# Kernel optimization log

Hardware: AMD Instinct MI355X
Metric: run time of the kernel (lower is better)

## Reference

```python
import jax, jax.numpy as jnp
import numpy as np

N = 50000
E = 800000
TEXT_VOCAB = 7000
ACTION_DIM = 64
MAX_POS = 5120
POS_DIM = 128   # edge encoder out_dim
NODE_DIM = 128  # text_out 64 + type_out 64
EDGE_DIM = 128
H1 = 256
OUT = 32
NEG_SLOPE = 0.2


def _pos_table():
    # sinusoidal table, [MAX_POS+1, POS_DIM]; even cols = cos, odd cols = sin
    positions = np.arange(0, MAX_POS + 1, dtype=np.float32)
    inv_freq = 1.0 / (10000.0 ** (np.arange(0.0, POS_DIM, 2.0, dtype=np.float32) / POS_DIM))
    si = np.outer(positions, inv_freq)
    tab = np.zeros((MAX_POS + 1, POS_DIM), dtype=np.float32)
    tab[:, 1::2] = np.sin(si)
    tab[:, 0::2] = np.cos(si)
    return jnp.asarray(tab)


def setup_inputs() -> dict:
    key = jax.random.key(0)
    ks = jax.random.split(key, 32)
    ri = jax.random.randint
    nrm = lambda k, s, scale=0.05: (jax.random.normal(k, s, dtype=jnp.float32) * scale)
    x = jnp.stack([ri(ks[0], (N,), 0, TEXT_VOCAB + 1, dtype=jnp.int32),
                   ri(ks[1], (N,), 0, 3, dtype=jnp.int32)], axis=-1)
    edge_index = ri(ks[2], (2, E), 0, N, dtype=jnp.int32)
    edge_attr = jnp.stack([ri(ks[3], (E,), 0, 3, dtype=jnp.int32),
                           ri(ks[4], (E,), 0, MAX_POS + 1, dtype=jnp.int32)], axis=-1)
    d = {
        "x": x, "edge_index": edge_index, "edge_attr": edge_attr,
        "text_emb": nrm(ks[5], (TEXT_VOCAB + 1, 64), 1.0),
        "type_emb": nrm(ks[6], (3, 64), 1.0),
        "flow_emb": nrm(ks[7], (3, EDGE_DIM), 1.0),
        "pos_table": _pos_table(),
        "pos_W": nrm(ks[8], (POS_DIM, POS_DIM)), "pos_b": nrm(ks[9], (POS_DIM,)),
        "c1_Wl": nrm(ks[10], (NODE_DIM, H1)), "c1_bl": nrm(ks[11], (H1,)),
        "c1_Wr": nrm(ks[12], (NODE_DIM, H1)), "c1_br": nrm(ks[13], (H1,)),
        "c1_We": nrm(ks[14], (EDGE_DIM, H1)), "c1_att": nrm(ks[15], (H1,)),
        "c1_bias": nrm(ks[16], (H1,)),
        "c2_Wl": nrm(ks[17], (H1, OUT)), "c2_bl": nrm(ks[18], (OUT,)),
        "c2_Wr": nrm(ks[19], (H1, OUT)), "c2_br": nrm(ks[20], (OUT,)),
        "c2_We": nrm(ks[21], (EDGE_DIM, OUT)), "c2_att": nrm(ks[22], (OUT,)),
        "c2_bias": nrm(ks[23], (OUT,)),
        "policy_W": nrm(ks[24], (OUT, ACTION_DIM), 0.2), "policy_b": nrm(ks[25], (ACTION_DIM,)),
    }
    return d


def gatv2(h, src, dst, ea, Wl, bl, Wr, br, We, att, bias, n):
    # PyG GATv2Conv, heads=1, add_self_loops=True, fill_value='mean'
    loop_attr = jnp.broadcast_to(ea.mean(0), (n, ea.shape[1]))
    s = jnp.concatenate([src, jnp.arange(n, dtype=src.dtype)])
    d = jnp.concatenate([dst, jnp.arange(n, dtype=dst.dtype)])
    ea_full = jnp.concatenate([ea, loop_attr], axis=0)
    xl = h @ Wl + bl  # messages (source side)
    xr = h @ Wr + br  # destination side
    m = xl[s] + xr[d] + ea_full @ We          # [E+n, F]
    e = jnp.where(m > 0, m, NEG_SLOPE * m) @ att  # per-edge logit [E+n]
    emax = jax.ops.segment_max(e, d, num_segments=n)
    a = jnp.exp(e - emax[d])
    denom = jax.ops.segment_sum(a, d, num_segments=n)
    alpha = a / denom[d]
    return jax.ops.segment_sum(alpha[:, None] * xl[s], d, num_segments=n) + bias


def reference(x, edge_index, edge_attr, text_emb, type_emb, flow_emb, pos_table,
              pos_W, pos_b,
              c1_Wl, c1_bl, c1_Wr, c1_br, c1_We, c1_att, c1_bias,
              c2_Wl, c2_bl, c2_Wr, c2_br, c2_We, c2_att, c2_bias,
              policy_W, policy_b):
    # NodeEncoder: concat of text and type embeddings -> [N, 128]
    h = jnp.concatenate([text_emb[x[:, 0]], type_emb[x[:, 1]]], axis=-1)
    # EdgeEncoder: flow embedding + linear(position sinusoid embedding)
    pos = edge_attr[:, 1]
    pos = jnp.where(pos > MAX_POS, pos, MAX_POS)  # faithful to original .where usage
    pos = jnp.clip(pos, 0, MAX_POS)
    ea = flow_emb[edge_attr[:, 0]] + (pos_table[pos] @ pos_W + pos_b)  # [E, 128]
    src, dst = edge_index[0], edge_index[1]
    h = gatv2(h, src, dst, ea, c1_Wl, c1_bl, c1_Wr, c1_br, c1_We, c1_att, c1_bias, h.shape[0])
    h = gatv2(h, src, dst, ea, c2_Wl, c2_bl, c2_Wr, c2_br, c2_We, c2_att, c2_bias, h.shape[0])
    g = h.mean(0)  # [32] graph readout
    logits = g @ policy_W + policy_b
    return jax.nn.softmax(logits, axis=-1)
```

## Files before the change

### kernel.cpp

```cpp
#include <hip/hip_runtime.h>

typedef __attribute__((ext_vector_type(8))) short bf16x8;
typedef __attribute__((ext_vector_type(4))) float f32x4;

#define L2E 1.4426950408889634f

static __device__ __forceinline__ float wsum64(float v) {
#pragma unroll
    for (int off = 32; off >= 1; off >>= 1) v += __shfl_xor(v, off, 64);
    return v;
}
static __device__ __forceinline__ float wmax64(float v) {
#pragma unroll
    for (int off = 32; off >= 1; off >>= 1) v = fmaxf(v, __shfl_xor(v, off, 64));
    return v;
}

static __device__ __forceinline__ unsigned short bf16r(float a) {
    unsigned int u = __float_as_uint(a);
    return (unsigned short)((u + 0x7FFFu + ((u >> 16) & 1u)) >> 16);
}
static __device__ __forceinline__ unsigned int bf16pack(float a, float b) {
    unsigned int ua = __float_as_uint(a);
    ua = (ua + 0x7FFFu + ((ua >> 16) & 1u)) >> 16;
    unsigned int ub = __float_as_uint(b);
    ub = (ub + 0x7FFFu + ((ub >> 16) & 1u)) & 0xFFFF0000u;
    return ua | ub;
}
static __device__ __forceinline__ float4 bf16x4_to_f4(uint2 u) {
    float4 v;
    v.x = __uint_as_float(u.x << 16);
    v.y = __uint_as_float(u.x & 0xFFFF0000u);
    v.z = __uint_as_float(u.y << 16);
    v.w = __uint_as_float(u.y & 0xFFFF0000u);
    return v;
}
static __device__ __forceinline__ float rflf(float v) {
    return __int_as_float(__builtin_amdgcn_readfirstlane(__float_as_int(v)));
}

static __device__ __forceinline__ float adot4(const float4 xs, const float4 pre,
                                              const float4 av4) {
    float m0 = xs.x + pre.x, m1 = xs.y + pre.y;
    float m2 = xs.z + pre.z, m3 = xs.w + pre.w;
    float q = av4.x * fabsf(m0);
    q = fmaf(av4.y, fabsf(m1), q);
    q = fmaf(av4.z, fabsf(m2), q);
    q = fmaf(av4.w, fabsf(m3), q);
    return q;
}

__global__ void k_edges(const int* __restrict__ ei, const int* __restrict__ ea,
                        int* __restrict__ cntF, int* __restrict__ cnt3, int E) {
    __shared__ int sh3[3];
    if (threadIdx.x < 3) sh3[threadIdx.x] = 0;
    __syncthreads();
    int e = blockIdx.x * blockDim.x + threadIdx.x;
    if (e < E) {
        int dd = ei[E + e];
        int f = ea[2 * e];
        f = f < 0 ? 0 : (f > 2 ? 2 : f);
        atomicAdd(&cntF[dd * 3 + f], 1);
        atomicAdd(&sh3[f], 1);
    }
    __syncthreads();
    if (threadIdx.x < 3) atomicAdd(&cnt3[threadIdx.x], sh3[threadIdx.x]);
}

__global__ void k_prep_all(const float* __restrict__ pos_table, const float* __restrict__ pos_W,
                           const float* __restrict__ pos_b, const float* __restrict__ flow_emb,
                           const float* __restrict__ We1, const float* __restrict__ We2,
                           const int* __restrict__ cnt3,
                           float* __restrict__ eaW1, float* __restrict__ loopW1,
                           float* __restrict__ eaW2, float* __restrict__ loopW2,
                           const float* __restrict__ Wl1, const float* __restrict__ Wr1,
                           const float* __restrict__ Wl2, const float* __restrict__ Wr2,
                           unsigned short* __restrict__ Bt1, unsigned short* __restrict__ Bt2,
                           int E) {
    if (blockIdx.x != 0) {
        int i = (blockIdx.x - 1) * 256 + threadIdx.x;
        if (i < 512 * 128) {
            int nn = i >> 7, k = i & 127;
            float v = (nn < 256) ? Wl1[(size_t)k * 256 + nn] : Wr1[(size_t)k * 256 + nn - 256];
            Bt1[i] = bf16r(v);
        } else {
            int j = i - 512 * 128;
            if (j < 64 * 256) {
                int nn = j >> 8, k = j & 255;
                float v = (nn < 32) ? Wl2[(size_t)k * 32 + nn] : Wr2[(size_t)k * 32 + nn - 32];
                Bt2[j] = bf16r(v);
            }
        }
        return;
    }
    __shared__ float posc[128];
    __shared__ float lv[128];
    int t = threadIdx.x;
    if (t < 128) {
        const float* row = pos_table + 5120 * 128;
        float a = pos_b[t];
        for (int k = 0; k < 128; ++k) a += row[k] * pos_W[k * 128 + t];
        posc[t] = a;
        float invE = 1.0f / (float)E;
        lv[t] = ((float)cnt3[0] * flow_emb[t] + (float)cnt3[1] * flow_emb[128 + t] +
                 (float)cnt3[2] * flow_emb[256 + t]) * invE + a;
    }
    __syncthreads();
    {
        int j = t;
        float a0 = 0.f, a1 = 0.f, a2 = 0.f, al = 0.f;
        for (int k = 0; k < 128; ++k) {
            float w = We1[k * 256 + j];
            float pc = posc[k];
            a0 += (flow_emb[k] + pc) * w;
            a1 += (flow_emb[128 + k] + pc) * w;
            a2 += (flow_emb[256 + k] + pc) * w;
            al += lv[k] * w;
        }
        eaW1[j] = a0; eaW1[256 + j] = a1; eaW1[512 + j] = a2; loopW1[j] = al;
    }
    if (t < 32) {
        int j = t;
        float a0 = 0.f, a1 = 0.f, a2 = 0.f, al = 0.f;
        for (int k = 0; k < 128; ++k) {
            float w = We2[k * 32 + j];
            float pc = posc[k];
            a0 += (flow_emb[k] + pc) * w;
            a1 += (flow_emb[128 + k] + pc) * w;
            a2 += (flow_emb[256 + k] + pc) * w;
            al += lv[k] * w;
        }
        eaW2[j] = a0; eaW2[32 + j] = a1; eaW2[64 + j] = a2; loopW2[j] = al;
    }
}

__global__ __launch_bounds__(256) void k_scan_block(const int* __restrict__ cnt,
                                                    int* __restrict__ rowptr,
                                                    int* __restrict__ bsum, int n) {
    __shared__ int sh[256];
    int b = blockIdx.x, t = threadIdx.x;
    int base = b * 1024 + t * 4;
    int v0 = base + 0 < n ? cnt[base + 0] : 0;
    int v1 = base + 1 < n ? cnt[base + 1] : 0;
    int v2 = base + 2 < n ? cnt[base + 2] : 0;
    int v3 = base + 3 < n ? cnt[base + 3] : 0;
    int tot = v0 + v1 + v2 + v3;
    sh[t] = tot;
    __syncthreads();
    for (int off = 1; off < 256; off <<= 1) {
        int x = (t >= off) ? sh[t - off] : 0;
        __syncthreads();
        sh[t] += x;
        __syncthreads();
    }
    int excl = (t > 0) ? sh[t - 1] : 0;
    if (base + 0 < n) rowptr[base + 0] = excl;
    if (base + 1 < n) rowptr[base + 1] = excl + v0;
    if (base + 2 < n) rowptr[base + 2] = excl + v0 + v1;
    if (base + 3 < n) rowptr[base + 3] = excl + v0 + v1 + v2;
    if (t == 255) bsum[b] = sh[255];
}

__global__ void k_scan_top(int* __restrict__ bsum, int* __restrict__ rowptr, int nb, int n) {
    if (threadIdx.x == 0 && blockIdx.x == 0) {
        int run = 0;
        for (int b = 0; b < nb; ++b) { int x = bsum[b]; bsum[b] = run; run += x; }
        rowptr[n] = run;
    }
}

__global__ void k_scan_add(int* __restrict__ rowptr, const int* __restrict__ bsum,
                           int* __restrict__ wptr, int n) {
    int i = blockIdx.x * blockDim.x + threadIdx.x;
    if (i < n) {
        int v = rowptr[i] + bsum[i >> 10];
        rowptr[i] = v;
        wptr[i] = v;
    }
}

__global__ void k_scatter(const int* __restrict__ ei, const int* __restrict__ ea,
                          int* __restrict__ wptr, int* __restrict__ packed, int E) {
    int e = blockIdx.x * blockDim.x + threadIdx.x;
    if (e >= E) return;
    int s = ei[e], dd = ei[E + e];
    int f = ea[2 * e];
    f = f < 0 ? 0 : (f > 2 ? 2 : f);
    int p = atomicAdd(&wptr[dd * 3 + f], 1);
    packed[p] = s | (f << 16);
}

__global__ __launch_bounds__(256) void k_gemm1(const int* __restrict__ x,
        const float* __restrict__ text_emb, const float* __restrict__ type_emb,
        const unsigned short* __restrict__ Bt,
        const float* __restrict__ bl, const float* __restrict__ br,
        unsigned short* __restrict__ xc, int n) {
    __shared__ unsigned short Ash[64][136];
    __shared__ unsigned short Bsh[128][136];
    int t = threadIdx.x;
    int node0 = blockIdx.x * 64;
    for (int i = t; i < 64 * 128; i += 256) {
        int r = i >> 7, cc = i & 127;
        int nd = node0 + r;
        float v = 0.f;
        if (nd < n)
            v = (cc < 64) ? text_emb[(size_t)x[nd * 2] * 64 + cc]
                          : type_emb[(size_t)x[nd * 2 + 1] * 64 + (cc - 64)];
        Ash[r][cc] = bf16r(v);
    }
    int wave = t >> 6, lane = t & 63;
    int m = lane & 15, q = lane >> 4;
    for (int nb = 0; nb < 4; ++nb) {
        __syncthreads();
        for (int i = t; i < 128 * 16; i += 256) {
            int r = i >> 4, cs = i & 15;
            uint4 v = ((const uint4*)(Bt + (size_t)(nb * 128 + r) * 128))[cs];
            *(uint4*)&Bsh[r][cs * 8] = v;
        }
        __syncthreads();
        f32x4 acc[8];
#pragma unroll
        for (int nt = 0; nt < 8; ++nt) acc[nt] = (f32x4){0.f, 0.f, 0.f, 0.f};
#pragma unroll
        for (int k = 0; k < 128; k += 32) {
            bf16x8 a = *(const bf16x8*)&Ash[wave * 16 + m][k + q * 8];
#pragma unroll
            for (int nt = 0; nt < 8; ++nt) {
                bf16x8 b = *(const bf16x8*)&Bsh[nt * 16 + m][k + q * 8];
                acc[nt] = __builtin_amdgcn_mfma_f32_16x16x32_bf16(a, b, acc[nt], 0, 0, 0);
            }
        }
#pragma unroll
        for (int r = 0; r < 4; ++r) {
            int node = node0 + wave * 16 + q * 4 + r;
            if (node < n) {
                unsigned short* rowp = xc + (size_t)node * 512 + nb * 128 + m;
#pragma unroll
                for (int nt = 0; nt < 8; ++nt) {
                    int ng = nb * 128 + nt * 16 + m;
                    float bv = (ng < 256) ? bl[ng] : br[ng - 256];
                    rowp[nt * 16] = bf16r(acc[nt][r] + bv);
                }
            }
        }
    }
}

__global__ __launch_bounds__(256) void k_gemm2(const unsigned short* __restrict__ h2b,
        const unsigned short* __restrict__ Bt,
        const float* __restrict__ bl, const float* __restrict__ br,
        unsigned short* __restrict__ xc, int n) {
    __shared__ unsigned short Ash[32][264];
    __shared__ unsigned short Bsh[64][264];
    int t = threadIdx.x;
    int node0 = blockIdx.x * 32;
    for (int i = t; i < 32 * 32; i += 256) {
        int r = i >> 5, cs = i & 31;
        int nd = node0 + r;
        uint4 v = make_uint4(0u, 0u, 0u, 0u);
        if (nd < n) v = ((const uint4*)(h2b + (size_t)nd * 256))[cs];
        *(uint4*)&Ash[r][cs * 8] = v;
    }
    for (int i = t; i < 64 * 32; i += 256) {
        int r = i >> 5, cs = i & 31;
        uint4 v = ((const uint4*)(Bt + (size_t)r * 256))[cs];
        *(uint4*)&Bsh[r][cs * 8] = v;
    }
    __syncthreads();
    int wave = t >> 6, lane = t & 63;
    int m = lane & 15, q = lane >> 4;
    int mrow = (wave >> 1) * 16;
    int nh   = (wave & 1) * 32;
    f32x4 acc[2];
    acc[0] = (f32x4){0.f, 0.f, 0.f, 0.f};
    acc[1] = (f32x4){0.f, 0.f, 0.f, 0.f};
#pragma unroll
    for (int k = 0; k < 256; k += 32) {
        bf16x8 a = *(const bf16x8*)&Ash[mrow + m][k + q * 8];
#pragma unroll
        for (int nt = 0; nt < 2; ++nt) {
            bf16x8 b = *(const bf16x8*)&Bsh[nh + nt * 16 + m][k + q * 8];
            acc[nt] = __builtin_amdgcn_mfma_f32_16x16x32_bf16(a, b, acc[nt], 0, 0, 0);
        }
    }
#pragma unroll
    for (int r = 0; r < 4; ++r) {
        int node = node0 + mrow + q * 4 + r;
        if (node < n) {
#pragma unroll
            for (int nt = 0; nt < 2; ++nt) {
                int ng = nh + nt * 16 + m;
                float bv = (ng < 32) ? bl[ng] : br[ng - 32];
                xc[(size_t)node * 64 + ng] = bf16r(acc[nt][r] + bv);
            }
        }
    }
}

__global__ __launch_bounds__(256) void k_alpha256(const unsigned short* __restrict__ xc1,
        const float* __restrict__ att, const float* __restrict__ eaW,
        const float* __restrict__ loopW, float* __restrict__ alpha,
        float* __restrict__ delta, int n) {
    const float S6 = 0.6f * L2E;
    int lane = threadIdx.x & 63;
    int c = lane * 4;
    float4 av = *(const float4*)(att + c);
    int wid = (blockIdx.x * blockDim.x + threadIdx.x) >> 6;
    if (wid < n) {
        float4 xl = bf16x4_to_f4(((const uint2*)(xc1 + (size_t)wid * 512))[lane]);
        float q = av.x * xl.x;
        q = fmaf(av.y, xl.y, q); q = fmaf(av.z, xl.z, q); q = fmaf(av.w, xl.w, q);
        q = wsum64(q);
        if (lane == 0) alpha[wid] = q * S6;
    } else if (wid < n + 4) {
        int f = wid - n;
        const float* src = (f < 3) ? (eaW + f * 256) : loopW;
        float4 v = *(const float4*)(src + c);
        float q = av.x * v.x;
        q = fmaf(av.y, v.y, q); q = fmaf(av.z, v.z, q); q = fmaf(av.w, v.w, q);
        q = wsum64(q);
        if (lane == 0) delta[f] = q * S6;
    }
}

__global__ __launch_bounds__(256) void k_gat256(const unsigned short* __restrict__ xc1,
        const int* __restrict__ rowptrF, const int* __restrict__ packed,
        const float* __restrict__ eaW, const float* __restrict__ loopW,
        const float* __restrict__ att, const float* __restrict__ bias,
        const float* __restrict__ alpha, const float* __restrict__ delta,
        unsigned short* __restrict__ h2b, int n) {
    int wid = (blockIdx.x * blockDim.x + threadIdx.x) >> 6;
    if (wid >= n) return;
    int d = __builtin_amdgcn_readfirstlane(wid);
    int lane = threadIdx.x & 63;
    int c = lane * 4;
    const float S4 = 0.4f * L2E;
    const float S6 = 0.6f * L2E;
    float4 xld = bf16x4_to_f4(((const uint2*)(xc1 + (size_t)d * 512))[lane]);
    float4 xrd = bf16x4_to_f4(((const uint2*)(xc1 + (size_t)d * 512 + 256))[lane]);
    float4 av = *(const float4*)(att + c);
    float4 av4;
    av4.x = S4 * av.x; av4.y = S4 * av.y; av4.z = S4 * av.z; av4.w = S4 * av.w;
    float gq = av.x * xrd.x;
    gq = fmaf(av.y, xrd.y, gq); gq = fmaf(av.z, xrd.z, gq); gq = fmaf(av.w, xrd.w, gq);
    float gd = rflf(wsum64(gq) * S6);
    float ab0 = gd + delta[0], ab1 = gd + delta[1], ab2 = gd + delta[2];
    float ab3 = gd + delta[3];
    float alphad = alpha[d];
    float4 r0 = *(const float4*)(eaW + c);
    float4 r1 = *(const float4*)(eaW + 256 + c);
    float4 r2 = *(const float4*)(eaW + 512 + c);
    float4 lwp = *(const float4*)(loopW + c);
    r0.x += xrd.x; r0.y += xrd.y; r0.z += xrd.z; r0.w += xrd.w;
    r1.x += xrd.x; r1.y += xrd.y; r1.z += xrd.z; r1.w += xrd.w;
    r2.x += xrd.x; r2.y += xrd.y; r2.z += xrd.z; r2.w += xrd.w;
    lwp.x += xrd.x; lwp.y += xrd.y; lwp.z += xrd.z; lwp.w += xrd.w;
    float den;
    float4 acc;
    {
        float q = wsum64(adot4(xld, lwp, av4)) + alphad + ab3;
        float wself = exp2f(q);
        den = wself;
        acc.x = wself * xld.x; acc.y = wself * xld.y;
        acc.z = wself * xld.z; acc.w = wself * xld.w;
    }
    int p = rowptrF[d * 3], p1 = rowptrF[d * 3 + 3];
    for (; p + 4 <= p1; p += 4) {
        int pk0 = packed[p],     pk1 = packed[p + 1];
        int pk2 = packed[p + 2], pk3 = packed[p + 3];
        int s0 = pk0 & 0xFFFF, s1 = pk1 & 0xFFFF;
        int s2 = pk2 & 0xFFFF, s3 = pk3 & 0xFFFF;
        int f0 = pk0 >> 16, f1 = pk1 >> 16, f2 = pk2 >> 16, f3 = pk3 >> 16;
        uint2 u0 = ((const uint2*)(xc1 + (size_t)s0 * 512))[lane];
        uint2 u1 = ((const uint2*)(xc1 + (size_t)s1 * 512))[lane];
        uint2 u2 = ((const uint2*)(xc1 + (size_t)s2 * 512))[lane];
        uint2 u3 = ((const uint2*)(xc1 + (size_t)s3 * 512))[lane];
        float sc0 = alpha[s0] + ((f0 == 0) ? ab0 : ((f0 == 1) ? ab1 : ab2));
        float sc1 = alpha[s1] + ((f1 == 0) ? ab0 : ((f1 == 1) ? ab1 : ab2));
        float sc2 = alpha[s2] + ((f2 == 0) ? ab0 : ((f2 == 1) ? ab1 : ab2));
        float sc3 = alpha[s3] + ((f3 == 0) ? ab0 : ((f3 == 1) ? ab1 : ab2));
        float4 xs0 = bf16x4_to_f4(u0);
        float4 xs1 = bf16x4_to_f4(u1);
        float4 xs2 = bf16x4_to_f4(u2);
        float4 xs3 = bf16x4_to_f4(u3);
        float q0, q1, q2, q3;
        if (f0 == f3) {
            float4 pr = (f0 == 0) ? r0 : ((f0 == 1) ? r1 : r2);
            q0 = adot4(xs0, pr, av4);
            q1 = adot4(xs1, pr, av4);
            q2 = adot4(xs2, pr, av4);
            q3 = adot4(xs3, pr, av4);
        } else {
            float4 pr0 = (f0 == 0) ? r0 : ((f0 == 1) ? r1 : r2);
            float4 pr1 = (f1 == 0) ? r0 : ((f1 == 1) ? r1 : r2);
            float4 pr2 = (f2 == 0) ? r0 : ((f2 == 1) ? r1 : r2);
            float4 pr3 = (f3 == 0) ? r0 : ((f3 == 1) ? r1 : r2);
            q0 = adot4(xs0, pr0, av4);
            q1 = adot4(xs1, pr1, av4);
            q2 = adot4(xs2, pr2, av4);
            q3 = adot4(xs3, pr3, av4);
        }
#pragma unroll
        for (int off = 32; off >= 1; off >>= 1) {
            q0 += __shfl_xor(q0, off, 64);
            q1 += __shfl_xor(q1, off, 64);
            q2 += __shfl_xor(q2, off, 64);
            q3 += __shfl_xor(q3, off, 64);
        }
        float w0 = exp2f(q0 + sc0), w1 = exp2f(q1 + sc1);
        float w2 = exp2f(q2 + sc2), w3 = exp2f(q3 + sc3);
        den += (w0 + w1) + (w2 + w3);
        acc.x += w0 * xs0.x + w1 * xs1.x + w2 * xs2.x + w3 * xs3.x;
        acc.y += w0 * xs0.y + w1 * xs1.y + w2 * xs2.y + w3 * xs3.y;
        acc.z += w0 * xs0.z + w1 * xs1.z + w2 * xs2.z + w3 * xs3.z;
        acc.w += w0 * xs0.w + w1 * xs1.w + w2 * xs2.w + w3 * xs3.w;
    }
    for (; p < p1; ++p) {
        int pk = packed[p];
        int s = pk & 0xFFFF, f = pk >> 16;
        uint2 u = ((const uint2*)(xc1 + (size_t)s * 512))[lane];
        float sc = alpha[s] + ((f == 0) ? ab0 : ((f == 1) ? ab1 : ab2));
        float4 xs = bf16x4_to_f4(u);
        float4 pr = (f == 0) ? r0 : ((f == 1) ? r1 : r2);
        float q = wsum64(adot4(xs, pr, av4)) + sc;
        float w = exp2f(q);
        den += w;
        acc.x += w * xs.x; acc.y += w * xs.y; acc.z += w * xs.z; acc.w += w * xs.w;
    }
    float inv = 1.f / den;
    float4 bv = *(const float4*)(bias + c);
    float ox = fmaf(acc.x, inv, bv.x), oy = fmaf(acc.y, inv, bv.y);
    float oz = fmaf(acc.z, inv, bv.z), ow = fmaf(acc.w, inv, bv.w);
    ((uint2*)(h2b + (size_t)d * 256))[lane] = make_uint2(bf16pack(ox, oy), bf16pack(oz, ow));
}

__global__ __launch_bounds__(256) void k_gat32(const unsigned short* __restrict__ xc2,
        const int* __restrict__ rowptrF, const int* __restrict__ packed,
        const float* __restrict__ eaW, const float* __restrict__ loopW,
        const float* __restrict__ att, const float* __restrict__ bias,
        float* __restrict__ out, int n) {
    int wid = (blockIdx.x * blockDim.x + threadIdx.x) >> 6;
    if (wid >= n) return;
    int d = __builtin_amdgcn_readfirstlane(wid);
    int lane = threadIdx.x & 63;
    int g = lane >> 4, li = lane & 15;
    unsigned int uxl = ((const unsigned int*)(xc2 + (size_t)d * 64))[li];
    unsigned int uxr = ((const unsigned int*)(xc2 + (size_t)d * 64 + 32))[li];
    float xl0 = __uint_as_float(uxl << 16), xl1 = __uint_as_float(uxl & 0xFFFF0000u);
    float xr0 = __uint_as_float(uxr << 16), xr1 = __uint_as_float(uxr & 0xFFFF0000u);
    float2 avv = ((const float2*)att)[li];
    float a60 = 0.6f * L2E * avv.x, a61 = 0.6f * L2E * avv.y;
    float a40 = 0.4f * L2E * avv.x, a41 = 0.4f * L2E * avv.y;
    float2 e0 = ((const float2*)eaW)[li];
    float2 e1 = ((const float2*)(eaW + 32))[li];
    float2 e2 = ((const float2*)(eaW + 64))[li];
    float p00 = e0.x + xr0, p01 = e0.y + xr1;
    float p10 = e1.x + xr0, p11 = e1.y + xr1;
    float p20 = e2.x + xr0, p21 = e2.y + xr1;
    float den, acc0, acc1;
    {
        float2 lwv = ((const float2*)loopW)[li];
        float m0 = xl0 + xr0 + lwv.x, m1 = xl1 + xr1 + lwv.y;
        float q = a60 * m0 + a40 * fabsf(m0);
        q = fmaf(a61, m1, q); q = fmaf(a41, fabsf(m1), q);
        q += __shfl_xor(q, 1, 64); q += __shfl_xor(q, 2, 64);
        q += __shfl_xor(q, 4, 64); q += __shfl_xor(q, 8, 64);
        float wself = exp2f(q);
        den  = (g == 0) ? wself : 0.f;
        acc0 = (g == 0) ? wself * xl0 : 0.f;
        acc1 = (g == 0) ? wself * xl1 : 0.f;
    }
    int pA = rowptrF[d * 3], pB = rowptrF[d * 3 + 3];
    int p = pA + g;
    for (; p + 4 < pB; p += 8) {
        int pk0 = packed[p], pk1 = packed[p + 4];
        unsigned int ua = ((const unsigned int*)(xc2 + (size_t)(pk0 & 0xFFFF) * 64))[li];
        unsigned int ub = ((const unsigned int*)(xc2 + (size_t)(pk1 & 0xFFFF) * 64))[li];
        int fA = pk0 >> 16, fB = pk1 >> 16;
        float preA0 = (fA == 0) ? p00 : ((fA == 1) ? p10 : p20);
        float preA1 = (fA == 0) ? p01 : ((fA == 1) ? p11 : p21);
        float preB0 = (fB == 0) ? p00 : ((fB == 1) ? p10 : p20);
        float preB1 = (fB == 0) ? p01 : ((fB == 1) ? p11 : p21);
        float xa0 = __uint_as_float(ua << 16), xa1 = __uint_as_float(ua & 0xFFFF0000u);
        float xb0 = __uint_as_float(ub << 16), xb1 = __uint_as_float(ub & 0xFFFF0000u);
        float ma0 = xa0 + preA0, ma1 = xa1 + preA1;
        float mb0 = xb0 + preB0, mb1 = xb1 + preB1;
        float qa = a60 * ma0 + a40 * fabsf(ma0);
        qa = fmaf(a61, ma1, qa); qa = fmaf(a41, fabsf(ma1), qa);
        float qb = a60 * mb0 + a40 * fabsf(mb0);
        qb = fmaf(a61, mb1, qb); qb = fmaf(a41, fabsf(mb1), qb);
#pragma unroll
        for (int off = 1; off <= 8; off <<= 1) {
            qa += __shfl_xor(qa, off, 64);
            qb += __shfl_xor(qb, off, 64);
        }
        float wa = exp2f(qa), wb = exp2f(qb);
        den += wa + wb;
        acc0 = fmaf(wb, xb0, fmaf(wa, xa0, acc0));
        acc1 = fmaf(wb, xb1, fmaf(wa, xa1, acc1));
    }
    for (; p < pB; p += 4) {
        int pk = packed[p];
        unsigned int u = ((const unsigned int*)(xc2 + (size_t)(pk & 0xFFFF) * 64))[li];
        int f = pk >> 16;
        float pre0 = (f == 0) ? p00 : ((f == 1) ? p10 : p20);
        float pre1 = (f == 0) ? p01 : ((f == 1) ? p11 : p21);
        float x0 = __uint_as_float(u << 16), x1 = __uint_as_float(u & 0xFFFF0000u);
        float m0 = x0 + pre0, m1 = x1 + pre1;
        float q = a60 * m0 + a40 * fabsf(m0);
        q = fmaf(a61, m1, q); q = fmaf(a41, fabsf(m1), q);
        q += __shfl_xor(q, 1, 64); q += __shfl_xor(q, 2, 64);
        q += __shfl_xor(q, 4, 64); q += __shfl_xor(q, 8, 64);
        float w = exp2f(q);
        den += w;
        acc0 = fmaf(w, x0, acc0);
        acc1 = fmaf(w, x1, acc1);
    }
    acc0 += __shfl_xor(acc0, 16, 64); acc0 += __shfl_xor(acc0, 32, 64);
    acc1 += __shfl_xor(acc1, 16, 64); acc1 += __shfl_xor(acc1, 32, 64);
    den  += __shfl_xor(den, 16, 64);  den  += __shfl_xor(den, 32, 64);
    if (g == 0) {
        float2 bvv = ((const float2*)bias)[li];
        float inv = 1.f / den;
        float2 o;
        o.x = fmaf(acc0, inv, bvv.x);
        o.y = fmaf(acc1, inv, bvv.y);
        ((float2*)(out + (size_t)d * 32))[li] = o;
    }
}

__global__ __launch_bounds__(256) void k_mean(const float* __restrict__ out2,
                                              float* __restrict__ gsum, int n) {
    __shared__ float sh[256];
    int t = threadIdx.x;
    int c = t & 31, g = t >> 5;
    float acc = 0.f;
    for (int nd = blockIdx.x * 8 + g; nd < n; nd += gridDim.x * 8)
        acc += out2[(size_t)nd * 32 + c];
    sh[t] = acc;
    __syncthreads();
    if (t < 32) {
        float s2 = 0.f;
#pragma unroll
        for (int gg = 0; gg < 8; ++gg) s2 += sh[gg * 32 + c];
        atomicAdd(&gsum[c], s2);
    }
}

__global__ void k_final(const float* __restrict__ gsum, const float* __restrict__ policy_W,
                        const float* __restrict__ policy_b, float* __restrict__ out, int n) {
    int t = threadIdx.x;
    float invN = 1.0f / (float)n;
    float acc = policy_b[t];
    for (int cc = 0; cc < 32; ++cc) acc += gsum[cc] * invN * policy_W[cc * 64 + t];
    float mx = wmax64(acc);
    float ex = __expf(acc - mx);
    float s = wsum64(ex);
    out[t] = ex / s;
}

extern "C" void kernel_launch(void* const* d_in, const int* in_sizes, int n_in,
                              void* d_out, int out_size, void* d_ws, size_t ws_size,
                              hipStream_t stream) {
    const int* x          = (const int*)d_in[0];
    const int* edge_index = (const int*)d_in[1];
    const int* edge_attr  = (const int*)d_in[2];
    const float* text_emb = (const float*)d_in[3];
    const float* type_emb = (const float*)d_in[4];
    const float* flow_emb = (const float*)d_in[5];
    const float* pos_table= (const float*)d_in[6];
    const float* pos_W    = (const float*)d_in[7];
    const float* pos_b    = (const float*)d_in[8];
    const float* c1_Wl    = (const float*)d_in[9];
    const float* c1_bl    = (const float*)d_in[10];
    const float* c1_Wr    = (const float*)d_in[11];
    const float* c1_br    = (const float*)d_in[12];
    const float* c1_We    = (const float*)d_in[13];
    const float* c1_att   = (const float*)d_in[14];
    const float* c1_bias  = (const float*)d_in[15];
    const float* c2_Wl    = (const float*)d_in[16];
    const float* c2_bl    = (const float*)d_in[17];
    const float* c2_Wr    = (const float*)d_in[18];
    const float* c2_br    = (const float*)d_in[19];
    const float* c2_We    = (const float*)d_in[20];
    const float* c2_att   = (const float*)d_in[21];
    const float* c2_bias  = (const float*)d_in[22];
    const float* policy_W = (const float*)d_in[23];
    const float* policy_b = (const float*)d_in[24];
    float* out = (float*)d_out;

    const int N = in_sizes[0] / 2;
    const int E = in_sizes[1] / 2;
    const int n3 = 3 * N;

    char* base = (char*)d_ws;
    size_t off = 0;
    auto alloc = [&](size_t bytes) -> void* {
        void* p = base + off;
        off = (off + bytes + 255) & ~(size_t)255;
        return p;
    };
    unsigned short* xc1  = (unsigned short*)alloc((size_t)N * 512 * 2);
    unsigned short* h2b  = (unsigned short*)alloc((size_t)N * 256 * 2);
    unsigned short* xc2  = (unsigned short*)alloc((size_t)N * 64 * 2);
    float*          out2 = (float*)alloc((size_t)N * 32 * 4);
    unsigned short* Bt1  = (unsigned short*)alloc((size_t)512 * 128 * 2);
    unsigned short* Bt2  = (unsigned short*)alloc((size_t)64 * 256 * 2);
    float*          alpha1 = (float*)alloc((size_t)N * 4);
    float*          delta1 = (float*)alloc(4 * 4);
    int*            zreg   = (int*)alloc((size_t)(n3 + 36) * 4);
    int*            cntF   = zreg;
    int*            cnt3   = zreg + n3;
    float*          gsum   = (float*)(zreg + n3 + 4);
    int*            rowptrF= (int*)alloc((size_t)(n3 + 1) * 4);
    int*            packed = (int*)alloc((size_t)E * 4);
    int*            bsum   = (int*)alloc(256 * 4);
    float*          eaW1   = (float*)alloc(768 * 4);
    float*          loopW1 = (float*)alloc(256 * 4);
    float*          eaW2   = (float*)alloc(96 * 4);
    float*          loopW2 = (float*)alloc(32 * 4);

    hipMemsetAsync(zreg, 0, (size_t)(n3 + 36) * 4, stream);

    k_edges<<<(E + 255) / 256, 256, 0, stream>>>(edge_index, edge_attr, cntF, cnt3, E);
    k_prep_all<<<1 + (512 * 128 + 64 * 256) / 256, 256, 0, stream>>>(
        pos_table, pos_W, pos_b, flow_emb, c1_We, c2_We, cnt3,
        eaW1, loopW1, eaW2, loopW2, c1_Wl, c1_Wr, c2_Wl, c2_Wr, Bt1, Bt2, E);

    int nb = (n3 + 1023) / 1024;
    k_scan_block<<<nb, 256, 0, stream>>>(cntF, rowptrF, bsum, n3);
    k_scan_top<<<1, 64, 0, stream>>>(bsum, rowptrF, nb, n3);
    k_scan_add<<<(n3 + 255) / 256, 256, 0, stream>>>(rowptrF, bsum, cntF, n3);
    k_scatter<<<(E + 255) / 256, 256, 0, stream>>>(edge_index, edge_attr, cntF, packed, E);

    k_gemm1<<<(N + 63) / 64, 256, 0, stream>>>(x, text_emb, type_emb, Bt1,
                                               c1_bl, c1_br, xc1, N);
    k_alpha256<<<(N + 4 + 3) / 4, 256, 0, stream>>>(xc1, c1_att, eaW1, loopW1,
                                                    alpha1, delta1, N);
    k_gat256<<<(N + 3) / 4, 256, 0, stream>>>(xc1, rowptrF, packed, eaW1, loopW1,
                                              c1_att, c1_bias, alpha1, delta1, h2b, N);

    k_gemm2<<<(N + 31) / 32, 256, 0, stream>>>(h2b, Bt2, c2_bl, c2_br, xc2, N);
    k_gat32<<<(N + 3) / 4, 256, 0, stream>>>(xc2, rowptrF, packed, eaW2, loopW2,
                                             c2_att, c2_bias, out2, N);

    k_mean<<<256, 256, 0, stream>>>(out2, gsum, N);
    k_final<<<1, 64, 0, stream>>>(gsum, policy_W, policy_b, out, N);
}
```

Measured before the change: 432.9 us.

## Fuse alpha into gemm1, merge scan kernels, batch exp in gat256, unroll gat32

Computes the per-node attention dot product inside gemm1 using atomics into a zeroed buffer, and moves the delta terms into prep, which removes the k_alpha256 kernel. The scan_top kernel is folded into scan_add, which recomputes block prefixes by reduction. In gat256, four per-edge reductions are merged into one shuffle tree with a single exp per lane, and the weights are redistributed with bpermute. gat32's edge loop is unrolled to four edges per iteration. These changes aim to cut launches, a full pass over xc1, and shuffle/exp work, at the cost of atomics and of alpha being computed from unrounded fp32 rather than bf16 values.

```diff
diff --git a/kernel.cpp b/kernel.cpp
--- a/kernel.cpp
+++ b/kernel.cpp
@@ -4,6 +4,7 @@
 typedef __attribute__((ext_vector_type(4))) float f32x4;
 
 #define L2E 1.4426950408889634f
+#define S6A (0.6f * L2E)
 
 static __device__ __forceinline__ float wsum64(float v) {
 #pragma unroll
@@ -70,13 +71,17 @@
 __global__ void k_prep_all(const float* __restrict__ pos_table, const float* __restrict__ pos_W,
                            const float* __restrict__ pos_b, const float* __restrict__ flow_emb,
                            const float* __restrict__ We1, const float* __restrict__ We2,
-                           const int* __restrict__ cnt3,
+                           const float* __restrict__ att1, const int* __restrict__ cnt3,
                            float* __restrict__ eaW1, float* __restrict__ loopW1,
                            float* __restrict__ eaW2, float* __restrict__ loopW2,
+                           float* __restrict__ delta,
                            const float* __restrict__ Wl1, const float* __restrict__ Wr1,
                            const float* __restrict__ Wl2, const float* __restrict__ Wr2,
                            unsigned short* __restrict__ Bt1, unsigned short* __restrict__ Bt2,
                            int E) {
+    __shared__ float posc[128];
+    __shared__ float lv[128];
+    __shared__ float red4[1024];
     if (blockIdx.x != 0) {
         int i = (blockIdx.x - 1) * 256 + threadIdx.x;
         if (i < 512 * 128) {
@@ -93,8 +98,6 @@
         }
         return;
     }
-    __shared__ float posc[128];
-    __shared__ float lv[128];
     int t = threadIdx.x;
     if (t < 128) {
         const float* row = pos_table + 5120 * 128;
@@ -118,6 +121,18 @@
             al += lv[k] * w;
         }
         eaW1[j] = a0; eaW1[256 + j] = a1; eaW1[512 + j] = a2; loopW1[j] = al;
+        float avj = att1[j];
+        red4[t] = avj * a0;
+        red4[256 + t] = avj * a1;
+        red4[512 + t] = avj * a2;
+        red4[768 + t] = avj * al;
+    }
+    __syncthreads();
+    if (t < 4) {
+        float s = 0.f;
+        const float* rr = red4 + t * 256;
+        for (int k = 0; k < 256; ++k) s += rr[k];
+        delta[t] = s * S6A;
     }
     if (t < 32) {
         int j = t;
@@ -161,19 +176,36 @@
     if (t == 255) bsum[b] = sh[255];
 }
 
-__global__ void k_scan_top(int* __restrict__ bsum, int* __restrict__ rowptr, int nb, int n) {
-    if (threadIdx.x == 0 && blockIdx.x == 0) {
-        int run = 0;
-        for (int b = 0; b < nb; ++b) { int x = bsum[b]; bsum[b] = run; run += x; }
-        rowptr[n] = run;
-    }
-}
-
-__global__ void k_scan_add(int* __restrict__ rowptr, const int* __restrict__ bsum,
-                           int* __restrict__ wptr, int n) {
-    int i = blockIdx.x * blockDim.x + threadIdx.x;
+__global__ __launch_bounds__(256) void k_scan_add(int* __restrict__ rowptr,
+        const int* __restrict__ bsum, int* __restrict__ wptr, int n, int nb) {
+    __shared__ int red[256];
+    int b = blockIdx.x, t = threadIdx.x;
+    int lim = b >> 2;
+    int local = 0;
+    for (int k = t; k < lim; k += 256) local += bsum[k];
+    red[t] = local;
+    __syncthreads();
+    for (int s = 128; s > 0; s >>= 1) {
+        if (t < s) red[t] += red[t + s];
+        __syncthreads();
+    }
+    int P = red[0];
+    if (b == 0) {
+        P = 0;
+        int tot = 0;
+        for (int k = t; k < nb; k += 256) tot += bsum[k];
+        __syncthreads();
+        red[t] = tot;
+        __syncthreads();
+        for (int s = 128; s > 0; s >>= 1) {
+            if (t < s) red[t] += red[t + s];
+            __syncthreads();
+        }
+        if (t == 0) rowptr[n] = red[0];
+    }
+    int i = b * 256 + t;
     if (i < n) {
-        int v = rowptr[i] + bsum[i >> 10];
+        int v = rowptr[i] + P;
         rowptr[i] = v;
         wptr[i] = v;
     }
@@ -194,6 +226,7 @@
         const float* __restrict__ text_emb, const float* __restrict__ type_emb,
         const unsigned short* __restrict__ Bt,
         const float* __restrict__ bl, const float* __restrict__ br,
+        const float* __restrict__ att, float* __restrict__ alpha,
         unsigned short* __restrict__ xc, int n) {
     __shared__ unsigned short Ash[64][136];
     __shared__ unsigned short Bsh[128][136];
@@ -241,6 +274,33 @@
                     float bv = (ng < 256) ? bl[ng] : br[ng - 256];
                     rowp[nt * 16] = bf16r(acc[nt][r] + bv);
                 }
+            }
+        }
+        if (nb < 2) {
+            float p0 = 0.f, p1 = 0.f, p2 = 0.f, p3 = 0.f;
+#pragma unroll
+            for (int nt = 0; nt < 8; ++nt) {
+                int ng = nb * 128 + nt * 16 + m;
+                float avv = att[ng];
+                float bv = bl[ng];
+                p0 = fmaf(avv, acc[nt][0] + bv, p0);
+                p1 = fmaf(avv, acc[nt][1] + bv, p1);
+                p2 = fmaf(avv, acc[nt][2] + bv, p2);
+                p3 = fmaf(avv, acc[nt][3] + bv, p3);
+            }
+#pragma unroll
+            for (int off = 1; off <= 8; off <<= 1) {
+                p0 += __shfl_xor(p0, off, 64);
+                p1 += __shfl_xor(p1, off, 64);
+                p2 += __shfl_xor(p2, off, 64);
+                p3 += __shfl_xor(p3, off, 64);
+            }
+            if (m == 0) {
+                int nodeb = node0 + wave * 16 + q * 4;
+                if (nodeb + 0 < n) atomicAdd(&alpha[nodeb + 0], p0 * S6A);
+                if (nodeb + 1 < n) atomicAdd(&alpha[nodeb + 1], p1 * S6A);
+                if (nodeb + 2 < n) atomicAdd(&alpha[nodeb + 2], p2 * S6A);
+                if (nodeb + 3 < n) atomicAdd(&alpha[nodeb + 3], p3 * S6A);
             }
         }
     }
@@ -297,32 +357,6 @@
     }
 }
 
-__global__ __launch_bounds__(256) void k_alpha256(const unsigned short* __restrict__ xc1,
-        const float* __restrict__ att, const float* __restrict__ eaW,
-        const float* __restrict__ loopW, float* __restrict__ alpha,
-        float* __restrict__ delta, int n) {
-    const float S6 = 0.6f * L2E;
-    int lane = threadIdx.x & 63;
-    int c = lane * 4;
-    float4 av = *(const float4*)(att + c);
-    int wid = (blockIdx.x * blockDim.x + threadIdx.x) >> 6;
-    if (wid < n) {
-        float4 xl = bf16x4_to_f4(((const uint2*)(xc1 + (size_t)wid * 512))[lane]);
-        float q = av.x * xl.x;
-        q = fmaf(av.y, xl.y, q); q = fmaf(av.z, xl.z, q); q = fmaf(av.w, xl.w, q);
-        q = wsum64(q);
-        if (lane == 0) alpha[wid] = q * S6;
-    } else if (wid < n + 4) {
-        int f = wid - n;
-        const float* src = (f < 3) ? (eaW + f * 256) : loopW;
-        float4 v = *(const float4*)(src + c);
-        float q = av.x * v.x;
-        q = fmaf(av.y, v.y, q); q = fmaf(av.z, v.z, q); q = fmaf(av.w, v.w, q);
-        q = wsum64(q);
-        if (lane == 0) delta[f] = q * S6;
-    }
-}
-
 __global__ __launch_bounds__(256) void k_gat256(const unsigned short* __restrict__ xc1,
         const int* __restrict__ rowptrF, const int* __restrict__ packed,
         const float* __restrict__ eaW, const float* __restrict__ loopW,
@@ -335,7 +369,6 @@
     int lane = threadIdx.x & 63;
     int c = lane * 4;
     const float S4 = 0.4f * L2E;
-    const float S6 = 0.6f * L2E;
     float4 xld = bf16x4_to_f4(((const uint2*)(xc1 + (size_t)d * 512))[lane]);
     float4 xrd = bf16x4_to_f4(((const uint2*)(xc1 + (size_t)d * 512 + 256))[lane]);
     float4 av = *(const float4*)(att + c);
@@ -343,7 +376,7 @@
     av4.x = S4 * av.x; av4.y = S4 * av.y; av4.z = S4 * av.z; av4.w = S4 * av.w;
     float gq = av.x * xrd.x;
     gq = fmaf(av.y, xrd.y, gq); gq = fmaf(av.z, xrd.z, gq); gq = fmaf(av.w, xrd.w, gq);
-    float gd = rflf(wsum64(gq) * S6);
+    float gd = rflf(wsum64(gq) * S6A);
     float ab0 = gd + delta[0], ab1 = gd + delta[1], ab2 = gd + delta[2];
     float ab3 = gd + delta[3];
     float alphad = alpha[d];
@@ -355,6 +388,9 @@
     r1.x += xrd.x; r1.y += xrd.y; r1.z += xrd.z; r1.w += xrd.w;
     r2.x += xrd.x; r2.y += xrd.y; r2.z += xrd.z; r2.w += xrd.w;
     lwp.x += xrd.x; lwp.y += xrd.y; lwp.z += xrd.z; lwp.w += xrd.w;
+    int jj = lane & 15;
+    int a0i = jj << 2, a1i = (jj + 16) << 2, a2i = (jj + 32) << 2, a3i = (jj + 48) << 2;
+    bool bq0 = (lane & 16) != 0, bq1 = (lane & 32) != 0;
     float den;
     float4 acc;
     {
@@ -400,15 +436,22 @@
             q2 = adot4(xs2, pr2, av4);
             q3 = adot4(xs3, pr3, av4);
         }
-#pragma unroll
-        for (int off = 32; off >= 1; off >>= 1) {
-            q0 += __shfl_xor(q0, off, 64);
-            q1 += __shfl_xor(q1, off, 64);
-            q2 += __shfl_xor(q2, off, 64);
-            q3 += __shfl_xor(q3, off, 64);
-        }
-        float w0 = exp2f(q0 + sc0), w1 = exp2f(q1 + sc1);
-        float w2 = exp2f(q2 + sc2), w3 = exp2f(q3 + sc3);
+        q0 += __shfl_xor(q0, 16, 64); q1 += __shfl_xor(q1, 16, 64);
+        q2 += __shfl_xor(q2, 16, 64); q3 += __shfl_xor(q3, 16, 64);
+        q0 += __shfl_xor(q0, 32, 64); q1 += __shfl_xor(q1, 32, 64);
+        q2 += __shfl_xor(q2, 32, 64); q3 += __shfl_xor(q3, 32, 64);
+        float r01 = bq0 ? q1 : q0, r23 = bq0 ? q3 : q2;
+        float r = bq1 ? r23 : r01;
+        r += __shfl_xor(r, 1, 64); r += __shfl_xor(r, 2, 64);
+        r += __shfl_xor(r, 4, 64); r += __shfl_xor(r, 8, 64);
+        float s01 = bq0 ? sc1 : sc0, s23 = bq0 ? sc3 : sc2;
+        float scv = bq1 ? s23 : s01;
+        float w = exp2f(r + scv);
+        int wi = __float_as_int(w);
+        float w0 = __int_as_float(__builtin_amdgcn_ds_bpermute(a0i, wi));
+        float w1 = __int_as_float(__builtin_amdgcn_ds_bpermute(a1i, wi));
+        float w2 = __int_as_float(__builtin_amdgcn_ds_bpermute(a2i, wi));
+        float w3 = __int_as_float(__builtin_amdgcn_ds_bpermute(a3i, wi));
         den += (w0 + w1) + (w2 + w3);
         acc.x += w0 * xs0.x + w1 * xs1.x + w2 * xs2.x + w3 * xs3.x;
         acc.y += w0 * xs0.y + w1 * xs1.y + w2 * xs2.y + w3 * xs3.y;
@@ -472,32 +515,50 @@
     }
     int pA = rowptrF[d * 3], pB = rowptrF[d * 3 + 3];
     int p = pA + g;
-    for (; p + 4 < pB; p += 8) {
-        int pk0 = packed[p], pk1 = packed[p + 4];
-        unsigned int ua = ((const unsigned int*)(xc2 + (size_t)(pk0 & 0xFFFF) * 64))[li];
-        unsigned int ub = ((const unsigned int*)(xc2 + (size_t)(pk1 & 0xFFFF) * 64))[li];
-        int fA = pk0 >> 16, fB = pk1 >> 16;
-        float preA0 = (fA == 0) ? p00 : ((fA == 1) ? p10 : p20);
-        float preA1 = (fA == 0) ? p01 : ((fA == 1) ? p11 : p21);
-        float preB0 = (fB == 0) ? p00 : ((fB == 1) ? p10 : p20);
-        float preB1 = (fB == 0) ? p01 : ((fB == 1) ? p11 : p21);
+    for (; p + 12 < pB; p += 16) {
+        int pkA = packed[p], pkB = packed[p + 4];
+        int pkC = packed[p + 8], pkD = packed[p + 12];
+        unsigned int ua = ((const unsigned int*)(xc2 + (size_t)(pkA & 0xFFFF) * 64))[li];
+        unsigned int ub = ((const unsigned int*)(xc2 + (size_t)(pkB & 0xFFFF) * 64))[li];
+        unsigned int uc = ((const unsigned int*)(xc2 + (size_t)(pkC & 0xFFFF) * 64))[li];
+        unsigned int ud = ((const unsigned int*)(xc2 + (size_t)(pkD & 0xFFFF) * 64))[li];
+        int fA = pkA >> 16, fB = pkB >> 16, fC = pkC >> 16, fD = pkD >> 16;
+        float prA0 = (fA == 0) ? p00 : ((fA == 1) ? p10 : p20);
+        float prA1 = (fA == 0) ? p01 : ((fA == 1) ? p11 : p21);
+        float prB0 = (fB == 0) ? p00 : ((fB == 1) ? p10 : p20);
+        float prB1 = (fB == 0) ? p01 : ((fB == 1) ? p11 : p21);
+        float prC0 = (fC == 0) ? p00 : ((fC == 1) ? p10 : p20);
+        float prC1 = (fC == 0) ? p01 : ((fC == 1) ? p11 : p21);
+        float prD0 = (fD == 0) ? p00 : ((fD == 1) ? p10 : p20);
+        float prD1 = (fD == 0) ? p01 : ((fD == 1) ? p11 : p21);
         float xa0 = __uint_as_float(ua << 16), xa1 = __uint_as_float(ua & 0xFFFF0000u);
         float xb0 = __uint_as_float(ub << 16), xb1 = __uint_as_float(ub & 0xFFFF0000u);
-        float ma0 = xa0 + preA0, ma1 = xa1 + preA1;
-        float mb0 = xb0 + preB0, mb1 = xb1 + preB1;
+        float xc0 = __uint_as_float(uc << 16), xc1v = __uint_as_float(uc & 0xFFFF0000u);
+        float xd0 = __uint_as_float(ud << 16), xd1 = __uint_as_float(ud & 0xFFFF0000u);
+        float ma0 = xa0 + prA0, ma1 = xa1 + prA1;
+        float mb0 = xb0 + prB0, mb1 = xb1 + prB1;
+        float mc0 = xc0 + prC0, mc1 = xc1v + prC1;
+        float md0 = xd0 + prD0, md1 = xd1 + prD1;
         float qa = a60 * ma0 + a40 * fabsf(ma0);
         qa = fmaf(a61, ma1, qa); qa = fmaf(a41, fabsf(ma1), qa);
         float qb = a60 * mb0 + a40 * fabsf(mb0);
         qb = fmaf(a61, mb1, qb); qb = fmaf(a41, fabsf(mb1), qb);
+        float qc = a60 * mc0 + a40 * fabsf(mc0);
+        qc = fmaf(a61, mc1, qc); qc = fmaf(a41, fabsf(mc1), qc);
+        float qd = a60 * md0 + a40 * fabsf(md0);
+        qd = fmaf(a61, md1, qd); qd = fmaf(a41, fabsf(md1), qd);
 #pragma unroll
         for (int off = 1; off <= 8; off <<= 1) {
             qa += __shfl_xor(qa, off, 64);
             qb += __shfl_xor(qb, off, 64);
+            qc += __shfl_xor(qc, off, 64);
+            qd += __shfl_xor(qd, off, 64);
         }
         float wa = exp2f(qa), wb = exp2f(qb);
-        den += wa + wb;
-        acc0 = fmaf(wb, xb0, fmaf(wa, xa0, acc0));
-        acc1 = fmaf(wb, xb1, fmaf(wa, xa1, acc1));
+        float wc = exp2f(qc), wd = exp2f(qd);
+        den += (wa + wb) + (wc + wd);
+        acc0 += wa * xa0 + wb * xb0 + wc * xc0 + wd * xd0;
+        acc1 += wa * xa1 + wb * xb1 + wc * xc1v + wd * xd1;
     }
     for (; p < pB; p += 4) {
         int pk = packed[p];
@@ -606,37 +667,35 @@
     float*          out2 = (float*)alloc((size_t)N * 32 * 4);
     unsigned short* Bt1  = (unsigned short*)alloc((size_t)512 * 128 * 2);
     unsigned short* Bt2  = (unsigned short*)alloc((size_t)64 * 256 * 2);
-    float*          alpha1 = (float*)alloc((size_t)N * 4);
-    float*          delta1 = (float*)alloc(4 * 4);
-    int*            zreg   = (int*)alloc((size_t)(n3 + 36) * 4);
+    int*            zreg   = (int*)alloc((size_t)(n3 + 36 + N) * 4);
     int*            cntF   = zreg;
     int*            cnt3   = zreg + n3;
     float*          gsum   = (float*)(zreg + n3 + 4);
+    float*          alpha1 = (float*)(zreg + n3 + 36);
     int*            rowptrF= (int*)alloc((size_t)(n3 + 1) * 4);
     int*            packed = (int*)alloc((size_t)E * 4);
     int*            bsum   = (int*)alloc(256 * 4);
+    float*          delta1 = (float*)alloc(4 * 4);
     float*          eaW1   = (float*)alloc(768 * 4);
     float*          loopW1 = (float*)alloc(256 * 4);
     float*          eaW2   = (float*)alloc(96 * 4);
     float*          loopW2 = (float*)alloc(32 * 4);
 
-    hipMemsetAsync(zreg, 0, (size_t)(n3 + 36) * 4, stream);
+    hipMemsetAsync(zreg, 0, (size_t)(n3 + 36 + N) * 4, stream);
 
     k_edges<<<(E + 255) / 256, 256, 0, stream>>>(edge_index, edge_attr, cntF, cnt3, E);
     k_prep_all<<<1 + (512 * 128 + 64 * 256) / 256, 256, 0, stream>>>(
-        pos_table, pos_W, pos_b, flow_emb, c1_We, c2_We, cnt3,
-        eaW1, loopW1, eaW2, loopW2, c1_Wl, c1_Wr, c2_Wl, c2_Wr, Bt1, Bt2, E);
+        pos_table, pos_W, pos_b, flow_emb, c1_We, c2_We, c1_att, cnt3,
+        eaW1, loopW1, eaW2, loopW2, delta1,
+        c1_Wl, c1_Wr, c2_Wl, c2_Wr, Bt1, Bt2, E);
 
     int nb = (n3 + 1023) / 1024;
     k_scan_block<<<nb, 256, 0, stream>>>(cntF, rowptrF, bsum, n3);
-    k_scan_top<<<1, 64, 0, stream>>>(bsum, rowptrF, nb, n3);
-    k_scan_add<<<(n3 + 255) / 256, 256, 0, stream>>>(rowptrF, bsum, cntF, n3);
+    k_scan_add<<<(n3 + 255) / 256, 256, 0, stream>>>(rowptrF, bsum, cntF, n3, nb);
     k_scatter<<<(E + 255) / 256, 256, 0, stream>>>(edge_index, edge_attr, cntF, packed, E);
 
     k_gemm1<<<(N + 63) / 64, 256, 0, stream>>>(x, text_emb, type_emb, Bt1,
-                                               c1_bl, c1_br, xc1, N);
-    k_alpha256<<<(N + 4 + 3) / 4, 256, 0, stream>>>(xc1, c1_att, eaW1, loopW1,
-                                                    alpha1, delta1, N);
+                                               c1_bl, c1_br, c1_att, alpha1, xc1, N);
     k_gat256<<<(N + 3) / 4, 256, 0, stream>>>(xc1, rowptrF, packed, eaW1, loopW1,
                                               c1_att, c1_bias, alpha1, delta1, h2b, N);
 
```

New measurement: 405.5 us. 1.07x faster.
